# Performance work log

Measured on AMD Instinct MI355X. Metric: run time of the kernel, lower is better.

Reference implementation:

```python
import jax, jax.numpy as jnp
import numpy as np

N_NODES = 100
K = 8
EPS = 1e-8

def gru_last_hidden(x_seq, Wih, Whh, bih, bhh):
    # x_seq: [T, N, F]; torch GRU gate order: r, z, n
    xW = jnp.einsum('tnf,gf->tng', x_seq, Wih) + bih  # [T, N, 3H]
    H = Whh.shape[1]
    def step(h, xw):
        hW = h @ Whh.T + bhh
        xr, xz, xn = jnp.split(xw, 3, axis=-1)
        hr, hz, hn = jnp.split(hW, 3, axis=-1)
        r = jax.nn.sigmoid(xr + hr)
        z = jax.nn.sigmoid(xz + hz)
        n = jnp.tanh(xn + r * hn)
        h_new = (1.0 - z) * n + z * h
        return h_new, None
    h0 = jnp.zeros((x_seq.shape[1], H), x_seq.dtype)
    hT, _ = jax.lax.scan(step, h0, xW)
    return hT  # [N, H]

def knn_edges(emb, k):
    # cosine sim, zero diagonal, top-k neighbors per row
    nrm = jnp.linalg.norm(emb, axis=1, keepdims=True)
    a = emb / jnp.maximum(nrm, EPS)
    sim = a @ a.T
    idx = jnp.arange(sim.shape[0])
    sim = sim.at[idx, idx].set(0.0)
    _, tgt = jax.lax.top_k(sim, k)               # [N, k]
    src = jnp.broadcast_to(idx[:, None], tgt.shape)
    return src.reshape(-1), tgt.reshape(-1)      # each [N*k]

def sage_conv(x, src, tgt, Wl, Wr, b):
    # PyG SAGEConv (mean aggr): lin_l(mean of neighbor msgs) + lin_r(x) + b
    msg = x[src]                                  # [E, D]
    agg = jax.ops.segment_sum(msg, tgt, num_segments=x.shape[0])
    cnt = jax.ops.segment_sum(jnp.ones((src.shape[0],), x.dtype), tgt,
                              num_segments=x.shape[0])
    agg = agg / jnp.maximum(cnt, 1.0)[:, None]
    return agg @ Wl.T + x @ Wr.T + b

def setup_inputs() -> dict:
    key = jax.random.key(0)
    ks = jax.random.split(key, 16)
    T, N, F, H = 2048, N_NODES, 128, 512
    EMB, FLAT_IN, FLAT_OUT = 128, 32, 64
    GIN = H + FLAT_OUT + EMB       # 704
    GH, GOUT = 256, 128
    OUT_IN = GOUT + H              # 640
    s = 0.02
    return {
        'node_feat': jax.random.normal(ks[0], (T, N, F), jnp.float32),
        'flat': jax.random.normal(ks[1], (N, FLAT_IN), jnp.float32),
        'emb': jax.random.normal(ks[2], (N, EMB), jnp.float32) * s,
        'gru_Wih': jax.random.normal(ks[3], (3 * H, F), jnp.float32) * s,
        'gru_Whh': jax.random.normal(ks[4], (3 * H, H), jnp.float32) * s,
        'gru_bih': jnp.zeros((3 * H,), jnp.float32),
        'gru_bhh': jnp.zeros((3 * H,), jnp.float32),
        'flat_W': jax.random.normal(ks[5], (FLAT_OUT, FLAT_IN), jnp.float32) * s,
        'flat_b': jnp.zeros((FLAT_OUT,), jnp.float32),
        'sage1_Wl': jax.random.normal(ks[6], (GH, GIN), jnp.float32) * s,
        'sage1_Wr': jax.random.normal(ks[7], (GH, GIN), jnp.float32) * s,
        'sage1_b': jnp.zeros((GH,), jnp.float32),
        'sage2_Wl': jax.random.normal(ks[8], (GOUT, GH), jnp.float32) * s,
        'sage2_Wr': jax.random.normal(ks[9], (GOUT, GH), jnp.float32) * s,
        'sage2_b': jnp.zeros((GOUT,), jnp.float32),
        'out_W': jax.random.normal(ks[10], (1, OUT_IN), jnp.float32) * s,
        'out_b': jnp.zeros((1,), jnp.float32),
    }

def reference(node_feat, flat, emb, gru_Wih, gru_Whh, gru_bih, gru_bhh,
              flat_W, flat_b, sage1_Wl, sage1_Wr, sage1_b,
              sage2_Wl, sage2_Wr, sage2_b, out_W, out_b):
    # node_feat arrives [T, N, F]; torch code transposes to [N, T, F] for a
    # batch_first encoder, which equals time-major scan over [T, N, F] here.
    enc_out = gru_last_hidden(node_feat, gru_Wih, gru_Whh, gru_bih, gru_bhh)  # [N, H]
    flat_e = flat @ flat_W.T + flat_b                                          # [N, 64]
    gnn_in = jnp.concatenate([enc_out, flat_e, emb], axis=-1)                  # [N, 704]
    src, tgt = knn_edges(jax.lax.stop_gradient(emb), K)
    h = jax.nn.relu(sage_conv(gnn_in, src, tgt, sage1_Wl, sage1_Wr, sage1_b))
    g = sage_conv(h, src, tgt, sage2_Wl, sage2_Wr, sage2_b)                    # [N, 128]
    out_feat = jnp.concatenate([g, enc_out], axis=-1)                          # [N, 640]
    out = jax.nn.sigmoid(out_feat @ out_W.T + out_b)
    return out.squeeze(-1)                                                      # [N]
```

## Files before the change

kernel.cpp:

```cpp
#include <hip/hip_runtime.h>
#include <math.h>

#define TS   2048
#define NN   100
#define FD   128
#define HD   512
#define G3   1536
#define NG   7
#define NSL  8
#define KNN  8
#define GIN  704
#define GH   256
#define GOUT 128

typedef float  f32x4  __attribute__((ext_vector_type(4)));
typedef __bf16 bf16x8 __attribute__((ext_vector_type(8)));
#define MFMA16(a, b, c) __builtin_amdgcn_mfma_f32_16x16x32_bf16((a), (b), (c), 0, 0, 0)

#define WXST 136

__device__ __forceinline__ float sig_(float v) {
    return __builtin_amdgcn_rcpf(1.f + __expf(-v));
}
__device__ __forceinline__ float tanh_(float v) {
    float e = __expf(2.f * v);
    return 1.f - 2.f * __builtin_amdgcn_rcpf(e + 1.f);
}


__device__ __forceinline__ void loadh8_lo(const __bf16* base, unsigned voff, f32x4* h) {
    asm volatile(
        "global_load_dwordx4 %0, %8, %9 sc0 sc1\n\t"
        "global_load_dwordx4 %1, %8, %9 offset:64 sc0 sc1\n\t"
        "global_load_dwordx4 %2, %8, %9 offset:128 sc0 sc1\n\t"
        "global_load_dwordx4 %3, %8, %9 offset:192 sc0 sc1\n\t"
        "global_load_dwordx4 %4, %8, %9 offset:256 sc0 sc1\n\t"
        "global_load_dwordx4 %5, %8, %9 offset:320 sc0 sc1\n\t"
        "global_load_dwordx4 %6, %8, %9 offset:384 sc0 sc1\n\t"
        "global_load_dwordx4 %7, %8, %9 offset:448 sc0 sc1\n\t"
        "s_waitcnt vmcnt(0)"
        : "=&v"(h[0]), "=&v"(h[1]), "=&v"(h[2]), "=&v"(h[3]),
          "=&v"(h[4]), "=&v"(h[5]), "=&v"(h[6]), "=&v"(h[7])
        : "v"(voff), "s"(base) : "memory");
}
__device__ __forceinline__ void loadh8_hi(const __bf16* base, unsigned voff, f32x4* h) {
    asm volatile(
        "global_load_dwordx4 %0, %8, %9 offset:512 sc0 sc1\n\t"
        "global_load_dwordx4 %1, %8, %9 offset:576 sc0 sc1\n\t"
        "global_load_dwordx4 %2, %8, %9 offset:640 sc0 sc1\n\t"
        "global_load_dwordx4 %3, %8, %9 offset:704 sc0 sc1\n\t"
        "global_load_dwordx4 %4, %8, %9 offset:768 sc0 sc1\n\t"
        "global_load_dwordx4 %5, %8, %9 offset:832 sc0 sc1\n\t"
        "global_load_dwordx4 %6, %8, %9 offset:896 sc0 sc1\n\t"
        "global_load_dwordx4 %7, %8, %9 offset:960 sc0 sc1\n\t"
        "s_waitcnt vmcnt(0)"
        : "=&v"(h[0]), "=&v"(h[1]), "=&v"(h[2]), "=&v"(h[3]),
          "=&v"(h[4]), "=&v"(h[5]), "=&v"(h[6]), "=&v"(h[7])
        : "v"(voff), "s"(base) : "memory");
}

__device__ __forceinline__ void storeh4_a(__bf16* base, unsigned voff,
                                          unsigned v0, unsigned v1, unsigned v2, unsigned v3) {
    asm volatile(
        "global_store_short %4, %0, %5 sc0 sc1\n\t"
        "global_store_short %4, %1, %5 offset:1024 sc0 sc1\n\t"
        "global_store_short %4, %2, %5 offset:2048 sc0 sc1\n\t"
        "global_store_short %4, %3, %5 offset:3072 sc0 sc1"
        :: "v"(v0), "v"(v1), "v"(v2), "v"(v3), "v"(voff), "s"(base) : "memory");
}

__device__ __forceinline__ void tagstore_a(int* base, unsigned voff, int val) {
    asm volatile("global_store_dword %1, %0, %2 sc0 sc1" :: "v"(val), "v"(voff), "s"(base) : "memory");
}
__device__ __forceinline__ int tagload_a(const int* base, unsigned voff) {
    int v;
    asm volatile("global_load_dword %0, %1, %2 sc0 sc1\n\ts_waitcnt vmcnt(0)"
                 : "=v"(v) : "v"(voff), "s"(base) : "memory");
    return v;
}

__device__ __forceinline__ bf16x8 cvt8(const float* p) {
    float4 a = *(const float4*)p, b = *(const float4*)(p + 4);
    bf16x8 r;
    r[0] = (__bf16)a.x; r[1] = (__bf16)a.y; r[2] = (__bf16)a.z; r[3] = (__bf16)a.w;
    r[4] = (__bf16)b.x; r[5] = (__bf16)b.y; r[6] = (__bf16)b.z; r[7] = (__bf16)b.w;
    return r;
}

__device__ void gru_loop(const float* __restrict__ x,
                         const float* __restrict__ Wih, const float* __restrict__ Whh,
                         const float* __restrict__ bih, const float* __restrict__ bhh,
                         __bf16* h0buf, __bf16* h1buf, float* enc, int* tags,
                         int g, int s, __bf16* WxP, __bf16* AxP)
{
    const int tid = threadIdx.x;
    const int w   = tid >> 6;
    const int ln  = tid & 63;
    const int nb  = g * 16;
    const int mi  = ln & 15;
    const int kq8 = (ln >> 4) * 8;
    const int cl  = 16 * w + mi;
    const int ch  = 64 * s + cl;

    for (int idx = tid; idx < 192 * 32; idx += 256) {
        int row = idx >> 5, c4 = idx & 31;
        int grow = (row >> 6) * HD + 64 * s + (row & 63);
        float4 v = ((const float4*)(Wih + (size_t)grow * FD))[c4];
        __bf16* d = WxP + row * WXST + c4 * 4;
        d[0] = (__bf16)v.x; d[1] = (__bf16)v.y; d[2] = (__bf16)v.z; d[3] = (__bf16)v.w;
    }

    bf16x8 wR[16], wZ[16], wN[16];
    {
        const float* pR = Whh + (size_t)ch * HD;
        const float* pZ = Whh + (size_t)(HD + ch) * HD;
        const float* pN = Whh + (size_t)(2 * HD + ch) * HD;
        #pragma unroll
        for (int kk = 0; kk < 16; ++kk) {
            int ko = 32 * kk + kq8;
            wR[kk] = cvt8(pR + ko);
            wZ[kk] = cvt8(pZ + ko);
            wN[kk] = cvt8(pN + ko);
        }
    }
    const float bR  = bih[ch] + bhh[ch];
    const float bZ  = bih[HD + ch] + bhh[HD + ch];
    const float bNX = bih[2 * HD + ch];
    const float bNH = bhh[2 * HD + ch];

    const int xrow  = tid >> 4;
    const int xnode = nb + xrow;
    const int xcol  = (tid & 15) * 8;

    {
        float4 xa = {0.f, 0.f, 0.f, 0.f}, xb = xa;
        if (xnode < NN) {
            const float* xp = x + (size_t)xnode * FD + xcol;
            xa = ((const float4*)xp)[0];
            xb = ((const float4*)xp)[1];
        }
        bf16x8 v;
        v[0] = (__bf16)xa.x; v[1] = (__bf16)xa.y; v[2] = (__bf16)xa.z; v[3] = (__bf16)xa.w;
        v[4] = (__bf16)xb.x; v[5] = (__bf16)xb.y; v[6] = (__bf16)xb.z; v[7] = (__bf16)xb.w;
        *(bf16x8*)(AxP + (size_t)xrow * WXST + xcol) = v;
    }
    __syncthreads();

    f32x4 accR = {0.f, 0.f, 0.f, 0.f}, accZ = accR, accNX = accR, accNH = accR;
    #pragma unroll
    for (int kk = 0; kk < 4; ++kk) {
        int ko = 32 * kk + kq8;
        bf16x8 av = *(const bf16x8*)(AxP + (size_t)mi * WXST + ko);
        accR  = MFMA16(av, *(const bf16x8*)(WxP + (size_t)cl * WXST + ko),         accR);
        accZ  = MFMA16(av, *(const bf16x8*)(WxP + (size_t)(64 + cl) * WXST + ko),  accZ);
        accNX = MFMA16(av, *(const bf16x8*)(WxP + (size_t)(128 + cl) * WXST + ko), accNX);
    }

    float hold[4] = {0.f, 0.f, 0.f, 0.f};

    const unsigned hv_voff = ((unsigned)(nb + mi) * HD + (unsigned)kq8) * 2u;
    const unsigned st_voff = ((unsigned)(nb + (ln >> 4) * 4) * HD + (unsigned)ch) * 2u;
    const unsigned tg_self = (unsigned)(g * NSL + s) * 64u;
    const unsigned tg_poll = (unsigned)(g * NSL + (ln & 7)) * 64u;

    #pragma unroll 1
    for (int t = 0; t < TS; ++t) {
        __bf16* hcur = (t & 1) ? h1buf : h0buf;
        __bf16* hnxt = (t & 1) ? h0buf : h1buf;

        float4 xa = {0.f, 0.f, 0.f, 0.f}, xb = xa;
        if (t + 1 < TS && xnode < NN) {
            const float* xp = x + ((size_t)(t + 1) * NN + xnode) * FD + xcol;
            xa = ((const float4*)xp)[0];
            xb = ((const float4*)xp)[1];
        }

        unsigned rdy = 0;
        do {
            int v = tagload_a(tags, tg_poll);
            rdy = (unsigned)(__ballot(v >= t) & 0xFFull);
        } while ((rdy & 0x0Fu) != 0x0Fu);

        f32x4 hv0[8];
        loadh8_lo(hcur, hv_voff, hv0);
        #pragma unroll
        for (int kk = 0; kk < 8; ++kk) {
            bf16x8 av = __builtin_bit_cast(bf16x8, hv0[kk]);
            accR  = MFMA16(av, wR[kk], accR);
            accZ  = MFMA16(av, wZ[kk], accZ);
            accNH = MFMA16(av, wN[kk], accNH);
        }

        while ((rdy & 0xF0u) != 0xF0u) {
            int v = tagload_a(tags, tg_poll);
            rdy = (unsigned)(__ballot(v >= t) & 0xFFull);
        }
        f32x4 hv1[8];
        loadh8_hi(hcur, hv_voff, hv1);
        #pragma unroll
        for (int kk = 0; kk < 8; ++kk) {
            bf16x8 av = __builtin_bit_cast(bf16x8, hv1[kk]);
            accR  = MFMA16(av, wR[8 + kk], accR);
            accZ  = MFMA16(av, wZ[8 + kk], accZ);
            accNH = MFMA16(av, wN[8 + kk], accNH);
        }

        unsigned pv[4];
        #pragma unroll
        for (int e = 0; e < 4; ++e) {
            float rv = sig_(accR[e] + bR);
            float zv = sig_(accZ[e] + bZ);
            float nv = tanh_(accNX[e] + bNX + rv * (accNH[e] + bNH));
            float hnew = (1.f - zv) * nv + zv * hold[e];
            hold[e] = hnew;
            pv[e] = (unsigned)__builtin_bit_cast(unsigned short, (__bf16)hnew);
        }
        storeh4_a(hnxt, st_voff, pv[0], pv[1], pv[2], pv[3]);
        asm volatile("s_waitcnt vmcnt(0)" ::: "memory");
        __syncthreads();
        if (tid == 0) tagstore_a(tags, tg_self, t + 1);

        const int nslot = (t + 1) & 1;
        if (t + 1 < TS) {
            bf16x8 v;
            v[0] = (__bf16)xa.x; v[1] = (__bf16)xa.y; v[2] = (__bf16)xa.z; v[3] = (__bf16)xa.w;
            v[4] = (__bf16)xb.x; v[5] = (__bf16)xb.y; v[6] = (__bf16)xb.z; v[7] = (__bf16)xb.w;
            *(bf16x8*)(AxP + ((size_t)nslot * 16 + xrow) * WXST + xcol) = v;
        }
        __syncthreads();

        accR = {0.f, 0.f, 0.f, 0.f}; accZ = accR; accNX = accR; accNH = accR;
        if (t + 1 < TS) {
            #pragma unroll
            for (int kk = 0; kk < 4; ++kk) {
                int ko = 32 * kk + kq8;
                bf16x8 av = *(const bf16x8*)(AxP + ((size_t)nslot * 16 + mi) * WXST + ko);
                accR  = MFMA16(av, *(const bf16x8*)(WxP + (size_t)cl * WXST + ko),         accR);
                accZ  = MFMA16(av, *(const bf16x8*)(WxP + (size_t)(64 + cl) * WXST + ko),  accZ);
                accNX = MFMA16(av, *(const bf16x8*)(WxP + (size_t)(128 + cl) * WXST + ko), accNX);
            }
        }
    }

    #pragma unroll
    for (int e = 0; e < 4; ++e) {
        int row = (ln >> 4) * 4 + e;
        if (nb + row < NN)
            enc[(size_t)(nb + row) * HD + ch] = hold[e];
    }
}

__global__ __launch_bounds__(256, 1) void gru_kernel(
    const float* __restrict__ x, const float* __restrict__ Wih,
    const float* __restrict__ Whh, const float* __restrict__ bih,
    const float* __restrict__ bhh,
    __bf16* h0buf, __bf16* h1buf, float* enc, int* sync)
{
    __shared__ __align__(16) __bf16 Wx[192 * WXST];
    __shared__ __align__(16) __bf16 Ax[2 * 16 * WXST];

    const int g = blockIdx.x >> 3;
    const int s = blockIdx.x & 7;

    gru_loop(x, Wih, Whh, bih, bhh, h0buf, h1buf, enc, sync, g, s, Wx, Ax);
}


__global__ void e1_gnn_in(const float* __restrict__ enc, const float* __restrict__ flat,
                          const float* __restrict__ emb, const float* __restrict__ fW,
                          const float* __restrict__ fb, float* __restrict__ gnn)
{
    int i = blockIdx.x, tid = threadIdx.x;
    const float4* src = (const float4*)(enc + (size_t)i * HD);
    float4* dst = (float4*)(gnn + (size_t)i * GIN);
    dst[tid] = src[tid];
    if (tid < 64) {
        float acc = fb[tid];
        const float* w  = fW + tid * 32;
        const float* fl = flat + i * 32;
        #pragma unroll
        for (int k = 0; k < 32; ++k) acc = fmaf(fl[k], w[k], acc);
        gnn[(size_t)i * GIN + HD + tid] = acc;
    }
    gnn[(size_t)i * GIN + HD + 64 + tid] = emb[(size_t)i * FD + tid];
}

__global__ void e2a_norm(const float* __restrict__ emb, float* __restrict__ mx)
{
    int j = threadIdx.x;
    if (j < NN) {
        float acc = 0.f;
        const float* e = emb + (size_t)j * FD;
        for (int d = 0; d < FD; ++d) acc = fmaf(e[d], e[d], acc);
        mx[j] = fmaxf(sqrtf(acc), 1e-8f);
    }
}

__global__ void e2b_knn(const float* __restrict__ emb, const float* __restrict__ mx,
                        int* __restrict__ tgt)
{
    int i = blockIdx.x, tid = threadIdx.x;
    __shared__ float ei[FD];
    __shared__ float srow[NN];
    ei[tid] = emb[(size_t)i * FD + tid];
    __syncthreads();
    if (tid < NN) {
        float acc = 0.f;
        const float* e = emb + (size_t)tid * FD;
        for (int d = 0; d < FD; ++d) acc = fmaf(ei[d], e[d], acc);
        float sim = acc / (mx[i] * mx[tid]);
        srow[tid] = (tid == i) ? 0.f : sim;
    }
    __syncthreads();
    if (tid == 0) {
        for (int t = 0; t < KNN; ++t) {
            float best = -1e30f; int bi = 0;
            for (int j = 0; j < NN; ++j) { float v = srow[j]; if (v > best) { best = v; bi = j; } }
            srow[bi] = -1e30f;
            tgt[i * KNN + t] = bi;
        }
    }
}

__global__ void e3_agg(const float* __restrict__ xin, const int* __restrict__ tgt,
                       float* __restrict__ agg, float* __restrict__ cnt, int D)
{
    int e = blockIdx.x, src = e >> 3, tg = tgt[e];
    for (int d = threadIdx.x; d < D; d += blockDim.x)
        atomicAdd(&agg[(size_t)tg * D + d], xin[(size_t)src * D + d]);
    if (threadIdx.x == 0) atomicAdd(&cnt[tg], 1.0f);
}

__global__ void e4_sage(const float* __restrict__ agg, const float* __restrict__ xin,
                        const float* __restrict__ cnt,
                        const float* __restrict__ Wl, const float* __restrict__ Wr,
                        const float* __restrict__ b, float* __restrict__ out,
                        int Din, int Dout, int dorelu)
{
    int j = blockIdx.x, o = threadIdx.x;
    extern __shared__ float sm[];
    float* la = sm;
    float* lx = sm + Din;
    for (int d = o; d < Din; d += blockDim.x) {
        la[d] = agg[(size_t)j * Din + d];
        lx[d] = xin[(size_t)j * Din + d];
    }
    __syncthreads();
    float inv = 1.f / fmaxf(cnt[j], 1.f);
    float acc1 = 0.f, acc2 = 0.f;
    const float* wl = Wl + (size_t)o * Din;
    const float* wr = Wr + (size_t)o * Din;
    for (int k = 0; k < Din; ++k) {
        acc1 = fmaf(la[k], wl[k], acc1);
        acc2 = fmaf(lx[k], wr[k], acc2);
    }
    float v = fmaf(acc1, inv, acc2) + b[o];
    if (dorelu) v = fmaxf(v, 0.f);
    out[(size_t)j * Dout + o] = v;
}

__global__ void e7_out(const float* __restrict__ g, const float* __restrict__ enc,
                       const float* __restrict__ oW, const float* __restrict__ ob,
                       float* __restrict__ out)
{
    int j = threadIdx.x;
    if (j < NN) {
        float acc = ob[0];
        const float* gr = g + (size_t)j * GOUT;
        for (int d = 0; d < GOUT; ++d) acc = fmaf(gr[d], oW[d], acc);
        const float* er = enc + (size_t)j * HD;
        for (int d = 0; d < HD; ++d) acc = fmaf(er[d], oW[GOUT + d], acc);
        out[j] = 1.f / (1.f + expf(-acc));
    }
}

extern "C" void kernel_launch(void* const* d_in, const int* in_sizes, int n_in,
                              void* d_out, int out_size, void* d_ws, size_t ws_size,
                              hipStream_t stream)
{
    const float* x    = (const float*)d_in[0];
    const float* flat = (const float*)d_in[1];
    const float* emb  = (const float*)d_in[2];
    const float* Wih  = (const float*)d_in[3];
    const float* Whh  = (const float*)d_in[4];
    const float* bih  = (const float*)d_in[5];
    const float* bhh  = (const float*)d_in[6];
    const float* fW   = (const float*)d_in[7];
    const float* fb   = (const float*)d_in[8];
    const float* s1Wl = (const float*)d_in[9];
    const float* s1Wr = (const float*)d_in[10];
    const float* s1b  = (const float*)d_in[11];
    const float* s2Wl = (const float*)d_in[12];
    const float* s2Wr = (const float*)d_in[13];
    const float* s2b  = (const float*)d_in[14];
    const float* oW   = (const float*)d_in[15];
    const float* ob   = (const float*)d_in[16];
    float* out = (float*)d_out;

    char* p = (char*)d_ws;
    __bf16* h0buf = (__bf16*)(p + 0);
    float*  agg1  = (float*)(p + 114688);
    float*  agg2  = (float*)(p + 396288);
    float*  cnt1  = (float*)(p + 498688);
    float*  cnt2  = (float*)(p + 499136);
    int*    sync  = (int*)  (p + 499584);
    __bf16* h1buf = (__bf16*)(p + 504192);
    float*  enc   = (float*)(p + 618880);
    float*  gnn   = (float*)(p + 848256);
    float*  h1s   = (float*)(p + 1129856);
    float*  gbuf  = (float*)(p + 1232256);
    float*  mx    = (float*)(p + 1283456);
    int*    tgt   = (int*)  (p + 1283904);

    (void)hipMemsetAsync(d_ws, 0, 504192, stream);

    gru_kernel<<<NG * NSL, 256, 0, stream>>>(x, Wih, Whh, bih, bhh, h0buf, h1buf, enc, sync);
    e1_gnn_in<<<NN, 128, 0, stream>>>(enc, flat, emb, fW, fb, gnn);
    e2a_norm<<<1, 128, 0, stream>>>(emb, mx);
    e2b_knn<<<NN, 128, 0, stream>>>(emb, mx, tgt);
    e3_agg<<<NN * KNN, 256, 0, stream>>>(gnn, tgt, agg1, cnt1, GIN);
    e4_sage<<<NN, GH, 2 * GIN * sizeof(float), stream>>>(agg1, gnn, cnt1, s1Wl, s1Wr, s1b, h1s, GIN, GH, 1);
    e3_agg<<<NN * KNN, 256, 0, stream>>>(h1s, tgt, agg2, cnt2, GH);
    e4_sage<<<NN, GOUT, 2 * GH * sizeof(float), stream>>>(agg2, h1s, cnt2, s2Wl, s2Wr, s2b, gbuf, GH, GOUT, 0);
    e7_out<<<1, 128, 0, stream>>>(gbuf, enc, oW, ob, out);
}
```

Before: 8.001 ms.

## Replace flag-based GRU step sync with timestep-tagged hidden-state words

Each hidden value is now stored as a 32-bit word holding the bf16 value in the low half and the timestep in the high half. Consumers poll the hidden-state data directly until every word carries the expected tag, which removes the separate tag store, the block-wide barrier and the store-drain wait per step. The cost is doubled hidden-state traffic, extra pack and validate ALU work, and possible repeated reloads of 512-byte chunks while spinning.

```diff
diff --git a/kernel.cpp b/kernel.cpp
--- a/kernel.cpp
+++ b/kernel.cpp
@@ -7,14 +7,16 @@
 #define HD   512
 #define G3   1536
 #define NG   7
+#define NPAD 112
 #define NSL  8
 #define KNN  8
 #define GIN  704
 #define GH   256
 #define GOUT 128
 
-typedef float  f32x4  __attribute__((ext_vector_type(4)));
-typedef __bf16 bf16x8 __attribute__((ext_vector_type(8)));
+typedef float    f32x4  __attribute__((ext_vector_type(4)));
+typedef unsigned u32x4  __attribute__((ext_vector_type(4)));
+typedef __bf16   bf16x8 __attribute__((ext_vector_type(8)));
 #define MFMA16(a, b, c) __builtin_amdgcn_mfma_f32_16x16x32_bf16((a), (b), (c), 0, 0, 0)
 
 #define WXST 136
@@ -28,55 +30,52 @@
 }
 
 
-__device__ __forceinline__ void loadh8_lo(const __bf16* base, unsigned voff, f32x4* h) {
+__device__ __forceinline__ void loadw8(const unsigned* base, unsigned voff, u32x4* h) {
     asm volatile(
         "global_load_dwordx4 %0, %8, %9 sc0 sc1\n\t"
-        "global_load_dwordx4 %1, %8, %9 offset:64 sc0 sc1\n\t"
+        "global_load_dwordx4 %1, %8, %9 offset:16 sc0 sc1\n\t"
         "global_load_dwordx4 %2, %8, %9 offset:128 sc0 sc1\n\t"
-        "global_load_dwordx4 %3, %8, %9 offset:192 sc0 sc1\n\t"
+        "global_load_dwordx4 %3, %8, %9 offset:144 sc0 sc1\n\t"
         "global_load_dwordx4 %4, %8, %9 offset:256 sc0 sc1\n\t"
-        "global_load_dwordx4 %5, %8, %9 offset:320 sc0 sc1\n\t"
+        "global_load_dwordx4 %5, %8, %9 offset:272 sc0 sc1\n\t"
         "global_load_dwordx4 %6, %8, %9 offset:384 sc0 sc1\n\t"
-        "global_load_dwordx4 %7, %8, %9 offset:448 sc0 sc1\n\t"
+        "global_load_dwordx4 %7, %8, %9 offset:400 sc0 sc1\n\t"
         "s_waitcnt vmcnt(0)"
         : "=&v"(h[0]), "=&v"(h[1]), "=&v"(h[2]), "=&v"(h[3]),
           "=&v"(h[4]), "=&v"(h[5]), "=&v"(h[6]), "=&v"(h[7])
         : "v"(voff), "s"(base) : "memory");
 }
-__device__ __forceinline__ void loadh8_hi(const __bf16* base, unsigned voff, f32x4* h) {
+
+__device__ __forceinline__ void storew4(unsigned* base, unsigned voff,
+                                        unsigned v0, unsigned v1, unsigned v2, unsigned v3) {
+    unsigned voff2 = voff + 4096u;
     asm volatile(
-        "global_load_dwordx4 %0, %8, %9 offset:512 sc0 sc1\n\t"
-        "global_load_dwordx4 %1, %8, %9 offset:576 sc0 sc1\n\t"
-        "global_load_dwordx4 %2, %8, %9 offset:640 sc0 sc1\n\t"
-        "global_load_dwordx4 %3, %8, %9 offset:704 sc0 sc1\n\t"
-        "global_load_dwordx4 %4, %8, %9 offset:768 sc0 sc1\n\t"
-        "global_load_dwordx4 %5, %8, %9 offset:832 sc0 sc1\n\t"
-        "global_load_dwordx4 %6, %8, %9 offset:896 sc0 sc1\n\t"
-        "global_load_dwordx4 %7, %8, %9 offset:960 sc0 sc1\n\t"
-        "s_waitcnt vmcnt(0)"
-        : "=&v"(h[0]), "=&v"(h[1]), "=&v"(h[2]), "=&v"(h[3]),
-          "=&v"(h[4]), "=&v"(h[5]), "=&v"(h[6]), "=&v"(h[7])
-        : "v"(voff), "s"(base) : "memory");
-}
-
-__device__ __forceinline__ void storeh4_a(__bf16* base, unsigned voff,
-                                          unsigned v0, unsigned v1, unsigned v2, unsigned v3) {
-    asm volatile(
-        "global_store_short %4, %0, %5 sc0 sc1\n\t"
-        "global_store_short %4, %1, %5 offset:1024 sc0 sc1\n\t"
-        "global_store_short %4, %2, %5 offset:2048 sc0 sc1\n\t"
-        "global_store_short %4, %3, %5 offset:3072 sc0 sc1"
-        :: "v"(v0), "v"(v1), "v"(v2), "v"(v3), "v"(voff), "s"(base) : "memory");
-}
-
-__device__ __forceinline__ void tagstore_a(int* base, unsigned voff, int val) {
-    asm volatile("global_store_dword %1, %0, %2 sc0 sc1" :: "v"(val), "v"(voff), "s"(base) : "memory");
-}
-__device__ __forceinline__ int tagload_a(const int* base, unsigned voff) {
-    int v;
-    asm volatile("global_load_dword %0, %1, %2 sc0 sc1\n\ts_waitcnt vmcnt(0)"
-                 : "=v"(v) : "v"(voff), "s"(base) : "memory");
-    return v;
+        "global_store_dword %4, %0, %6 sc0 sc1\n\t"
+        "global_store_dword %4, %1, %6 offset:2048 sc0 sc1\n\t"
+        "global_store_dword %5, %2, %6 sc0 sc1\n\t"
+        "global_store_dword %5, %3, %6 offset:2048 sc0 sc1"
+        :: "v"(v0), "v"(v1), "v"(v2), "v"(v3), "v"(voff), "v"(voff2), "s"(base) : "memory");
+}
+
+__device__ __forceinline__ bool valid8(const u32x4* hw, unsigned tt) {
+    unsigned ok = 1u;
+    #pragma unroll
+    for (int q = 0; q < 8; ++q) {
+        ok &= (unsigned)((hw[q][0] >> 16) == tt);
+        ok &= (unsigned)((hw[q][1] >> 16) == tt);
+        ok &= (unsigned)((hw[q][2] >> 16) == tt);
+        ok &= (unsigned)((hw[q][3] >> 16) == tt);
+    }
+    return __all((int)ok);
+}
+
+__device__ __forceinline__ bf16x8 pack8(u32x4 a, u32x4 b) {
+    u32x4 r;
+    r[0] = (a[0] & 0xffffu) | (a[1] << 16);
+    r[1] = (a[2] & 0xffffu) | (a[3] << 16);
+    r[2] = (b[0] & 0xffffu) | (b[1] << 16);
+    r[3] = (b[2] & 0xffffu) | (b[3] << 16);
+    return __builtin_bit_cast(bf16x8, r);
 }
 
 __device__ __forceinline__ bf16x8 cvt8(const float* p) {
@@ -90,7 +89,7 @@
 __device__ void gru_loop(const float* __restrict__ x,
                          const float* __restrict__ Wih, const float* __restrict__ Whh,
                          const float* __restrict__ bih, const float* __restrict__ bhh,
-                         __bf16* h0buf, __bf16* h1buf, float* enc, int* tags,
+                         unsigned* h0buf, unsigned* h1buf, float* enc,
                          int g, int s, __bf16* WxP, __bf16* AxP)
 {
     const int tid = threadIdx.x;
@@ -158,15 +157,14 @@
 
     float hold[4] = {0.f, 0.f, 0.f, 0.f};
 
-    const unsigned hv_voff = ((unsigned)(nb + mi) * HD + (unsigned)kq8) * 2u;
-    const unsigned st_voff = ((unsigned)(nb + (ln >> 4) * 4) * HD + (unsigned)ch) * 2u;
-    const unsigned tg_self = (unsigned)(g * NSL + s) * 64u;
-    const unsigned tg_poll = (unsigned)(g * NSL + (ln & 7)) * 64u;
+    const unsigned hv_voff = ((unsigned)(nb + mi) * HD + (unsigned)kq8) * 4u;
+    const unsigned st_voff = ((unsigned)(nb + (ln >> 4) * 4) * HD + (unsigned)ch) * 4u;
 
     #pragma unroll 1
     for (int t = 0; t < TS; ++t) {
-        __bf16* hcur = (t & 1) ? h1buf : h0buf;
-        __bf16* hnxt = (t & 1) ? h0buf : h1buf;
+        unsigned* hcur = (t & 1) ? h1buf : h0buf;
+        unsigned* hnxt = (t & 1) ? h0buf : h1buf;
+        const unsigned tt = (unsigned)t;
 
         float4 xa = {0.f, 0.f, 0.f, 0.f}, xb = xa;
         if (t + 1 < TS && xnode < NN) {
@@ -175,37 +173,22 @@
             xb = ((const float4*)xp)[1];
         }
 
-        unsigned rdy = 0;
-        do {
-            int v = tagload_a(tags, tg_poll);
-            rdy = (unsigned)(__ballot(v >= t) & 0xFFull);
-        } while ((rdy & 0x0Fu) != 0x0Fu);
-
-        f32x4 hv0[8];
-        loadh8_lo(hcur, hv_voff, hv0);
         #pragma unroll
-        for (int kk = 0; kk < 8; ++kk) {
-            bf16x8 av = __builtin_bit_cast(bf16x8, hv0[kk]);
-            accR  = MFMA16(av, wR[kk], accR);
-            accZ  = MFMA16(av, wZ[kk], accZ);
-            accNH = MFMA16(av, wN[kk], accNH);
-        }
-
-        while ((rdy & 0xF0u) != 0xF0u) {
-            int v = tagload_a(tags, tg_poll);
-            rdy = (unsigned)(__ballot(v >= t) & 0xFFull);
-        }
-        f32x4 hv1[8];
-        loadh8_hi(hcur, hv_voff, hv1);
-        #pragma unroll
-        for (int kk = 0; kk < 8; ++kk) {
-            bf16x8 av = __builtin_bit_cast(bf16x8, hv1[kk]);
-            accR  = MFMA16(av, wR[8 + kk], accR);
-            accZ  = MFMA16(av, wZ[8 + kk], accZ);
-            accNH = MFMA16(av, wN[8 + kk], accNH);
-        }
-
-        unsigned pv[4];
+        for (int c = 0; c < 4; ++c) {
+            u32x4 hw[8];
+            unsigned vo = hv_voff + 512u * (unsigned)c;
+            do { loadw8(hcur, vo, hw); } while (!valid8(hw, tt));
+            #pragma unroll
+            for (int kk = 0; kk < 4; ++kk) {
+                bf16x8 av = pack8(hw[2 * kk], hw[2 * kk + 1]);
+                accR  = MFMA16(av, wR[4 * c + kk], accR);
+                accZ  = MFMA16(av, wZ[4 * c + kk], accZ);
+                accNH = MFMA16(av, wN[4 * c + kk], accNH);
+            }
+        }
+
+        const unsigned tagn = (unsigned)(t + 1) << 16;
+        unsigned pw[4];
         #pragma unroll
         for (int e = 0; e < 4; ++e) {
             float rv = sig_(accR[e] + bR);
@@ -213,12 +196,9 @@
             float nv = tanh_(accNX[e] + bNX + rv * (accNH[e] + bNH));
             float hnew = (1.f - zv) * nv + zv * hold[e];
             hold[e] = hnew;
-            pv[e] = (unsigned)__builtin_bit_cast(unsigned short, (__bf16)hnew);
-        }
-        storeh4_a(hnxt, st_voff, pv[0], pv[1], pv[2], pv[3]);
-        asm volatile("s_waitcnt vmcnt(0)" ::: "memory");
-        __syncthreads();
-        if (tid == 0) tagstore_a(tags, tg_self, t + 1);
+            pw[e] = tagn | (unsigned)__builtin_bit_cast(unsigned short, (__bf16)hnew);
+        }
+        storew4(hnxt, st_voff, pw[0], pw[1], pw[2], pw[3]);
 
         const int nslot = (t + 1) & 1;
         if (t + 1 < TS) {
@@ -254,7 +234,7 @@
     const float* __restrict__ x, const float* __restrict__ Wih,
     const float* __restrict__ Whh, const float* __restrict__ bih,
     const float* __restrict__ bhh,
-    __bf16* h0buf, __bf16* h1buf, float* enc, int* sync)
+    unsigned* h0buf, unsigned* h1buf, float* enc)
 {
     __shared__ __align__(16) __bf16 Wx[192 * WXST];
     __shared__ __align__(16) __bf16 Ax[2 * 16 * WXST];
@@ -262,7 +242,7 @@
     const int g = blockIdx.x >> 3;
     const int s = blockIdx.x & 7;
 
-    gru_loop(x, Wih, Whh, bih, bhh, h0buf, h1buf, enc, sync, g, s, Wx, Ax);
+    gru_loop(x, Wih, Whh, bih, bhh, h0buf, h1buf, enc, g, s, Wx, Ax);
 }
 
 
@@ -398,23 +378,22 @@
     float* out = (float*)d_out;
 
     char* p = (char*)d_ws;
-    __bf16* h0buf = (__bf16*)(p + 0);
-    float*  agg1  = (float*)(p + 114688);
-    float*  agg2  = (float*)(p + 396288);
-    float*  cnt1  = (float*)(p + 498688);
-    float*  cnt2  = (float*)(p + 499136);
-    int*    sync  = (int*)  (p + 499584);
-    __bf16* h1buf = (__bf16*)(p + 504192);
-    float*  enc   = (float*)(p + 618880);
-    float*  gnn   = (float*)(p + 848256);
-    float*  h1s   = (float*)(p + 1129856);
-    float*  gbuf  = (float*)(p + 1232256);
-    float*  mx    = (float*)(p + 1283456);
-    int*    tgt   = (int*)  (p + 1283904);
-
-    (void)hipMemsetAsync(d_ws, 0, 504192, stream);
-
-    gru_kernel<<<NG * NSL, 256, 0, stream>>>(x, Wih, Whh, bih, bhh, h0buf, h1buf, enc, sync);
+    unsigned* h0buf = (unsigned*)(p + 0);
+    unsigned* h1buf = (unsigned*)(p + 229376);
+    float*    agg1  = (float*)(p + 458752);
+    float*    agg2  = (float*)(p + 740352);
+    float*    cnt1  = (float*)(p + 842752);
+    float*    cnt2  = (float*)(p + 843200);
+    float*    enc   = (float*)(p + 843648);
+    float*    gnn   = (float*)(p + 1073024);
+    float*    h1s   = (float*)(p + 1354624);
+    float*    gbuf  = (float*)(p + 1457024);
+    float*    mx    = (float*)(p + 1508224);
+    int*      tgt   = (int*)  (p + 1508672);
+
+    (void)hipMemsetAsync(d_ws, 0, 843648, stream);
+
+    gru_kernel<<<NG * NSL, 256, 0, stream>>>(x, Wih, Whh, bih, bhh, h0buf, h1buf, enc);
     e1_gnn_in<<<NN, 128, 0, stream>>>(enc, flat, emb, fW, fb, gnn);
     e2a_norm<<<1, 128, 0, stream>>>(emb, mx);
     e2b_knn<<<NN, 128, 0, stream>>>(emb, mx, tgt);
```

After: 11.59 ms. 1.45x slower.
